# Kernel tuning notes

Measured on AMD Instinct MI355X. Metric: run time of the kernel, lower is better.

Reference implementation:

```python
import jax, jax.numpy as jnp
import numpy as np

EMB = 128
HEADS = 8
B = 8
T = 2048


def setup_inputs() -> dict:
    key = jax.random.key(0)
    ks = jax.random.split(key, 6)
    x = jax.random.normal(ks[0], (B, T, EMB), dtype=jnp.float32)
    # torch Linear(emb, heads*emb, bias=False): store as (in, out) so y = x @ W
    scale = 1.0 / np.sqrt(EMB)
    Wq = jax.random.uniform(ks[1], (EMB, HEADS * EMB), jnp.float32, -scale, scale)
    Wk = jax.random.uniform(ks[2], (EMB, HEADS * EMB), jnp.float32, -scale, scale)
    Wv = jax.random.uniform(ks[3], (EMB, HEADS * EMB), jnp.float32, -scale, scale)
    so = 1.0 / np.sqrt(HEADS * EMB)
    Wo = jax.random.uniform(ks[4], (HEADS * EMB, EMB), jnp.float32, -so, so)
    bo = jax.random.uniform(ks[5], (EMB,), jnp.float32, -so, so)
    return {"x": x, "Wq": Wq, "Wk": Wk, "Wv": Wv, "Wo": Wo, "bo": bo}


def reference(x, Wq, Wk, Wv, Wo, bo):
    b, t, e = x.shape
    h = HEADS
    q = (x @ Wq).reshape(b, t, h, e)  # [b,t,h,e]
    k = (x @ Wk).reshape(b, t, h, e)
    v = (x @ Wv).reshape(b, t, h, e)
    # scores: [b,h,q,k], scaled by sqrt(e) (per-head dim == emb here)
    scores = jnp.einsum('bqhe,bkhe->bhqk', q, k) / jnp.sqrt(jnp.asarray(e, x.dtype))
    attn = jax.nn.softmax(scores, axis=-1)
    out = jnp.einsum('bhqk,bkhe->bqhe', attn, v).reshape(b, t, h * e)
    return out @ Wo + bo
```

## Files before the change

kernel.cpp:

```cpp
#include <hip/hip_runtime.h>

using bf16x8 = __attribute__((ext_vector_type(8))) short;
using f32x4  = __attribute__((ext_vector_type(4))) float;

__device__ __forceinline__ ushort f2bf(float f) {
    union { float f; unsigned int u; } c; c.f = f;
    unsigned int u = c.u;
    u = (u + 0x7fffu + ((u >> 16) & 1u)) >> 16;
    return (ushort)u;
}

#if defined(__has_builtin)
#if __has_builtin(__builtin_amdgcn_cvt_pk_bf16_f32)
#define HAS_PK_BF16 1
#endif
#endif
__device__ __forceinline__ unsigned int pkbf(float a, float b) {
#ifdef HAS_PK_BF16
    typedef __bf16 bf2 __attribute__((ext_vector_type(2)));
    union { bf2 v; unsigned int u; } cv;
    cv.v = __builtin_amdgcn_cvt_pk_bf16_f32(a, b);
    return cv.u;
#else
    return (unsigned int)f2bf(a) | ((unsigned int)f2bf(b) << 16);
#endif
}

__device__ __forceinline__ void dma16(const ushort* g, ushort* l) {
    __builtin_amdgcn_global_load_lds(
        (const __attribute__((address_space(1))) unsigned int*)g,
        (__attribute__((address_space(3))) unsigned int*)l, 16, 0, 0);
}

constexpr int BB   = 8;
constexpr int HH   = 8;
constexpr int TT   = 2048;
constexpr int DD   = 128;
#define C2F (0.08838834764831845f * 1.4426950408889634f)

__global__ void prep_kernel(const float* __restrict__ x,
                            const float* __restrict__ Wq, const float* __restrict__ Wk,
                            const float* __restrict__ Wv, const float* __restrict__ Wo,
                            ushort* __restrict__ xb, ushort* __restrict__ WqkvT,
                            ushort* __restrict__ WoT) {
    int t = blockIdx.x * 256 + threadIdx.x;
    if (t < 524288) {
        float4 v = ((const float4*)x)[t];
        ushort4 o;
        o.x = f2bf(v.x); o.y = f2bf(v.y); o.z = f2bf(v.z); o.w = f2bf(v.w);
        ((ushort4*)xb)[t] = o;
    } else if (t < 524288 + 393216) {
        int i = t - 524288;
        int j = i >> 7, kk = i & 127;
        const float* W = (j < 1024) ? Wq : ((j < 2048) ? Wk : Wv);
        int jj = j & 1023;
        WqkvT[j * 128 + kk] = f2bf(W[kk * 1024 + jj]);
    } else {
        int i = t - 917504;
        int e = i >> 10, kk = i & 1023;
        WoT[e * 1024 + kk] = f2bf(Wo[kk * 128 + e]);
    }
}

__global__ __launch_bounds__(256, 2)
void qkv_gemm(const ushort* __restrict__ xb, const ushort* __restrict__ WqkvT,
              ushort* __restrict__ q, ushort* __restrict__ k, ushort* __restrict__ vt) {
    __shared__ ushort Al[128 * 136];
    __shared__ ushort Bl[128 * 136];
    const int tid = threadIdx.x;
    const int n0 = blockIdx.x * 128, m0 = blockIdx.y * 128;

    for (int s = tid; s < 2048; s += 256) {
        int row = s >> 4, oct = s & 15;
        *(uint4*)&Al[row * 136 + oct * 8] = *(const uint4*)&xb[m0 * 128 + s * 8];
        *(uint4*)&Bl[row * 136 + oct * 8] = *(const uint4*)&WqkvT[n0 * 128 + s * 8];
    }
    __syncthreads();

    const int w = tid >> 6, lane = tid & 63, l15 = lane & 15, g = lane >> 4;
    const int wm = (w & 1) * 64, wn = (w >> 1) * 64;
    f32x4 acc[4][4] = {};

#pragma unroll
    for (int ks = 0; ks < 4; ks++) {
        bf16x8 af[4], bfr[4];
#pragma unroll
        for (int mb = 0; mb < 4; mb++)
            af[mb] = *(const bf16x8*)&Al[(wm + mb * 16 + l15) * 136 + ks * 32 + g * 8];
#pragma unroll
        for (int nb = 0; nb < 4; nb++)
            bfr[nb] = *(const bf16x8*)&Bl[(wn + nb * 16 + l15) * 136 + ks * 32 + g * 8];
#pragma unroll
        for (int mb = 0; mb < 4; mb++)
#pragma unroll
            for (int nb = 0; nb < 4; nb++)
                acc[mb][nb] = __builtin_amdgcn_mfma_f32_16x16x32_bf16(af[mb], bfr[nb], acc[mb][nb], 0, 0, 0);
    }

    const int which = n0 >> 10;
    const int b = m0 >> 11;
    const int h = (n0 >> 7) & 7;
    const int bh = b * HH + h;
    if (which == 0) {
#pragma unroll
        for (int mb = 0; mb < 4; mb++)
#pragma unroll
            for (int nb = 0; nb < 4; nb++)
#pragma unroll
                for (int r = 0; r < 4; r++) {
                    int t = (m0 + wm + mb * 16 + g * 4 + r) & 2047;
                    int e = wn + nb * 16 + l15;
                    q[((size_t)bh * TT + t) * DD + e] = f2bf(acc[mb][nb][r]);
                }
    } else if (which == 1) {
#pragma unroll
        for (int mb = 0; mb < 4; mb++)
#pragma unroll
            for (int nb = 0; nb < 4; nb++)
#pragma unroll
                for (int r = 0; r < 4; r++) {
                    int t = (m0 + wm + mb * 16 + g * 4 + r) & 2047;
                    int e = wn + nb * 16 + l15;
                    int esw = ((((e >> 3) ^ (t & 7)) << 3) | (e & 7));
                    k[((size_t)bh * TT + t) * DD + esw] = f2bf(acc[mb][nb][r]);
                }
    } else {
        __syncthreads();
        ushort* Tl = Al;
#pragma unroll
        for (int mb = 0; mb < 4; mb++)
#pragma unroll
            for (int nb = 0; nb < 4; nb++)
#pragma unroll
                for (int r = 0; r < 4; r++)
                    Tl[(wn + nb * 16 + l15) * 136 + wm + mb * 16 + g * 4 + r] = f2bf(acc[mb][nb][r]);
        __syncthreads();
        const int c0 = (m0 & 2047) >> 5;
        for (int s = tid; s < 2048; s += 256) {
            int e = s >> 4, x = s & 15;
            int cl = x >> 2, pos = x & 3;
            int el = e & 15;
            int vsw = (el ^ (el >> 2)) & 3;
            int tsrc = cl * 32 + ((pos ^ vsw) * 8);
            uint4 val = *(const uint4*)&Tl[e * 136 + tsrc];
            *(uint4*)&vt[(size_t)(((bh * 64 + c0 + cl) * 128) + e) * 32 + pos * 8] = val;
        }
    }
}

__global__ __launch_bounds__(256, 2)
void attn_kernel(const ushort* __restrict__ q, const ushort* __restrict__ k,
                 const ushort* __restrict__ vt, ushort* __restrict__ ao) {
    __shared__ ushort Kl[2][32 * 128];
    __shared__ ushort Vl[2][128 * 32];
    __shared__ ushort Pl[4 * 64 * 32];

    const int idx = blockIdx.x;
    const int qt256 = idx & 7, h = (idx >> 3) & 7, b = idx >> 6;
    const int t0 = qt256 * 256;
    const int bh = b * HH + h;
    const ushort* qg  = q  + (size_t)bh * TT * DD;
    const ushort* kg  = k  + (size_t)bh * TT * DD;
    const ushort* vtg = vt + (size_t)bh * 64 * DD * 32;

    const int tid = threadIdx.x, w = tid >> 6, lane = tid & 63;
    const int l15 = lane & 15, g = lane >> 4;
    const int swk = l15 & 7;
    const int swv = (l15 ^ (l15 >> 2)) & 3;

    bf16x8 qf[4][4];
#pragma unroll
    for (int qt = 0; qt < 4; qt++)
#pragma unroll
        for (int ks = 0; ks < 4; ks++)
            qf[qt][ks] = *(const bf16x8*)&qg[(size_t)(t0 + w * 64 + qt * 16 + l15) * DD + ks * 32 + g * 8];

    const int seg = tid * 8;
#pragma unroll
    for (int j = 0; j < 2; j++) {
        dma16(kg  + seg + j * 2048, &Kl[0][seg + j * 2048]);
        dma16(vtg + seg + j * 2048, &Vl[0][seg + j * 2048]);
    }

    f32x4 o[4][8] = {};
    float ls[4] = {0.0f, 0.0f, 0.0f, 0.0f};

    for (int c = 0; c < 64; c++) {
        const int cur = c & 1;
        __syncthreads();

        if (c < 63) {
            const ushort* kn = kg  + (size_t)(c + 1) * 4096;
            const ushort* vn = vtg + (size_t)(c + 1) * 4096;
#pragma unroll
            for (int j = 0; j < 2; j++) {
                dma16(kn + seg + j * 2048, &Kl[cur ^ 1][seg + j * 2048]);
                dma16(vn + seg + j * 2048, &Vl[cur ^ 1][seg + j * 2048]);
            }
        }

#pragma unroll
        for (int kt = 0; kt < 2; kt++) {
            f32x4 st[4] = {};
#pragma unroll
            for (int ks = 0; ks < 4; ks++) {
                bf16x8 kf = *(const bf16x8*)&Kl[cur][(kt * 16 + l15) * 128 + (((ks * 4 + g) ^ swk) * 8)];
#pragma unroll
                for (int qt = 0; qt < 4; qt++)
                    st[qt] = __builtin_amdgcn_mfma_f32_16x16x32_bf16(kf, qf[qt][ks], st[qt], 0, 0, 0);
            }
            const int kb = 2 * kt + (g >> 1);
#pragma unroll
            for (int qt = 0; qt < 4; qt++) {
                float p0 = __builtin_amdgcn_exp2f(st[qt][0] * C2F);
                float p1 = __builtin_amdgcn_exp2f(st[qt][1] * C2F);
                float p2 = __builtin_amdgcn_exp2f(st[qt][2] * C2F);
                float p3 = __builtin_amdgcn_exp2f(st[qt][3] * C2F);
                ls[qt] += (p0 + p1) + (p2 + p3);
                uint2 pk;
                pk.x = pkbf(p0, p1);
                pk.y = pkbf(p2, p3);
                *(uint2*)&Pl[w * 2048 + (qt * 16 + l15) * 32 + ((kb ^ swv) * 8) + (g & 1) * 4] = pk;
            }
        }

        {
            bf16x8 pa[4];
#pragma unroll
            for (int qt = 0; qt < 4; qt++)
                pa[qt] = *(const bf16x8*)&Pl[w * 2048 + (qt * 16 + l15) * 32 + ((g ^ swv) * 8)];
#pragma unroll
            for (int eb = 0; eb < 8; eb++) {
                bf16x8 vb = *(const bf16x8*)&Vl[cur][(eb * 16 + l15) * 32 + ((g ^ swv) * 8)];
#pragma unroll
                for (int qt = 0; qt < 4; qt++)
                    o[qt][eb] = __builtin_amdgcn_mfma_f32_16x16x32_bf16(pa[qt], vb, o[qt][eb], 0, 0, 0);
            }
        }
    }

#pragma unroll
    for (int qt = 0; qt < 4; qt++) {
        float tot = ls[qt];
        tot += __shfl_xor(tot, 16);
        tot += __shfl_xor(tot, 32);
        float inv[4];
#pragma unroll
        for (int r = 0; r < 4; r++)
            inv[r] = 1.0f / __shfl(tot, g * 4 + r, 64);
#pragma unroll
        for (int eb = 0; eb < 8; eb++)
#pragma unroll
            for (int r = 0; r < 4; r++) {
                int m = t0 + w * 64 + qt * 16 + g * 4 + r;
                int col = h * 128 + eb * 16 + l15;
                ao[(size_t)(b * TT + m) * 1024 + col] = f2bf(o[qt][eb][r] * inv[r]);
            }
    }
}

__global__ __launch_bounds__(256, 2)
void outproj_gemm(const ushort* __restrict__ ao, const ushort* __restrict__ WoT,
                  const float* __restrict__ bo, float* __restrict__ out) {
    __shared__ ushort Al[64 * 72];
    __shared__ ushort Bl[64 * 72];
    const int tid = threadIdx.x;
    const int n0 = blockIdx.x * 64, m0 = blockIdx.y * 64;
    const int w = tid >> 6, lane = tid & 63, l15 = lane & 15, g = lane >> 4;
    const int wm = (w & 1) * 32, wn = (w >> 1) * 32;
    f32x4 acc[2][2] = {};

    for (int kc = 0; kc < 16; kc++) {
        int k0 = kc * 64;
        __syncthreads();
        for (int s = tid; s < 512; s += 256) {
            int row = s >> 3, oct = s & 7;
            *(uint4*)&Al[row * 72 + oct * 8] = *(const uint4*)&ao[(size_t)(m0 + row) * 1024 + k0 + oct * 8];
            *(uint4*)&Bl[row * 72 + oct * 8] = *(const uint4*)&WoT[(n0 + row) * 1024 + k0 + oct * 8];
        }
        __syncthreads();
#pragma unroll
        for (int ks = 0; ks < 2; ks++) {
            bf16x8 af[2], bfr[2];
#pragma unroll
            for (int mb = 0; mb < 2; mb++)
                af[mb] = *(const bf16x8*)&Al[(wm + mb * 16 + l15) * 72 + ks * 32 + g * 8];
#pragma unroll
            for (int nb = 0; nb < 2; nb++)
                bfr[nb] = *(const bf16x8*)&Bl[(wn + nb * 16 + l15) * 72 + ks * 32 + g * 8];
#pragma unroll
            for (int mb = 0; mb < 2; mb++)
#pragma unroll
                for (int nb = 0; nb < 2; nb++)
                    acc[mb][nb] = __builtin_amdgcn_mfma_f32_16x16x32_bf16(af[mb], bfr[nb], acc[mb][nb], 0, 0, 0);
        }
    }

#pragma unroll
    for (int mb = 0; mb < 2; mb++)
#pragma unroll
        for (int nb = 0; nb < 2; nb++) {
            int j = n0 + wn + nb * 16 + l15;
            float bias = bo[j];
#pragma unroll
            for (int r = 0; r < 4; r++) {
                int m = m0 + wm + mb * 16 + g * 4 + r;
                out[(size_t)m * 128 + j] = acc[mb][nb][r] + bias;
            }
        }
}

extern "C" void kernel_launch(void* const* d_in, const int* in_sizes, int n_in,
                              void* d_out, int out_size, void* d_ws, size_t ws_size,
                              hipStream_t stream) {
    const float* x  = (const float*)d_in[0];
    const float* Wq = (const float*)d_in[1];
    const float* Wk = (const float*)d_in[2];
    const float* Wv = (const float*)d_in[3];
    const float* Wo = (const float*)d_in[4];
    const float* bo = (const float*)d_in[5];
    float* out = (float*)d_out;

    char* ws = (char*)d_ws;
    ushort* xb    = (ushort*)(ws);
    ushort* WqkvT = (ushort*)(ws + 4194304);
    ushort* WoT   = (ushort*)(ws + 4980736);
    ushort* qb    = (ushort*)(ws + 5242880);
    ushort* kb    = (ushort*)(ws + 38797312);
    ushort* vtb   = (ushort*)(ws + 72351744);
    ushort* ao    = (ushort*)(ws + 105906176);

    prep_kernel<<<4096, 256, 0, stream>>>(x, Wq, Wk, Wv, Wo, xb, WqkvT, WoT);
    qkv_gemm<<<dim3(24, 128), 256, 0, stream>>>(xb, WqkvT, qb, kb, vtb);
    attn_kernel<<<512, 256, 0, stream>>>(qb, kb, vtb, ao);
    outproj_gemm<<<dim3(2, 256), 256, 0, stream>>>(ao, WoT, bo, out);
}
```

Before: 274.3 us.

## Switch attention to 32x32x16 MFMA with register-resident P via permlane32 swap

Rewrites the attention inner loop to use 32x32x16 bf16 MFMA tiles instead of 16x16x32, so the S-to-P accumulator layout can feed the PV MFMA directly after a permlane32 swap, removing the per-chunk LDS round trip for P. The softmax scale is folded into Q during the projection kernel, which removes a multiply per score. It also adds s_setprio around the MFMA sections and drops the P shared buffer, which reduces LDS usage. The risk is higher register pressure from the 16-wide accumulators and reliance on the permlane32 swap instruction layout being correct.

```diff
diff --git a/kernel.cpp b/kernel.cpp
--- a/kernel.cpp
+++ b/kernel.cpp
@@ -2,6 +2,7 @@
 
 using bf16x8 = __attribute__((ext_vector_type(8))) short;
 using f32x4  = __attribute__((ext_vector_type(4))) float;
+using f32x16 = __attribute__((ext_vector_type(16))) float;
 
 __device__ __forceinline__ ushort f2bf(float f) {
     union { float f; unsigned int u; } c; c.f = f;
@@ -13,6 +14,9 @@
 #if defined(__has_builtin)
 #if __has_builtin(__builtin_amdgcn_cvt_pk_bf16_f32)
 #define HAS_PK_BF16 1
+#endif
+#if __has_builtin(__builtin_amdgcn_permlane32_swap)
+#define HAS_PL32 1
 #endif
 #endif
 __device__ __forceinline__ unsigned int pkbf(float a, float b) {
@@ -23,6 +27,16 @@
     return cv.u;
 #else
     return (unsigned int)f2bf(a) | ((unsigned int)f2bf(b) << 16);
+#endif
+}
+
+__device__ __forceinline__ void pl32swap(unsigned &a, unsigned &b) {
+#ifdef HAS_PL32
+    typedef unsigned uint2v __attribute__((ext_vector_type(2)));
+    uint2v r = __builtin_amdgcn_permlane32_swap(a, b, false, false);
+    a = r.x; b = r.y;
+#else
+    asm volatile("v_permlane32_swap_b32 %0, %1" : "+v"(a), "+v"(b));
 #endif
 }
 
@@ -110,7 +124,7 @@
                 for (int r = 0; r < 4; r++) {
                     int t = (m0 + wm + mb * 16 + g * 4 + r) & 2047;
                     int e = wn + nb * 16 + l15;
-                    q[((size_t)bh * TT + t) * DD + e] = f2bf(acc[mb][nb][r]);
+                    q[((size_t)bh * TT + t) * DD + e] = f2bf(acc[mb][nb][r] * C2F);
                 }
     } else if (which == 1) {
 #pragma unroll
@@ -153,7 +167,6 @@
                  const ushort* __restrict__ vt, ushort* __restrict__ ao) {
     __shared__ ushort Kl[2][32 * 128];
     __shared__ ushort Vl[2][128 * 32];
-    __shared__ ushort Pl[4 * 64 * 32];
 
     const int idx = blockIdx.x;
     const int qt256 = idx & 7, h = (idx >> 3) & 7, b = idx >> 6;
@@ -164,16 +177,16 @@
     const ushort* vtg = vt + (size_t)bh * 64 * DD * 32;
 
     const int tid = threadIdx.x, w = tid >> 6, lane = tid & 63;
-    const int l15 = lane & 15, g = lane >> 4;
-    const int swk = l15 & 7;
+    const int l31 = lane & 31, hi = lane >> 5, l15 = lane & 15;
+    const int swk = lane & 7;
     const int swv = (l15 ^ (l15 >> 2)) & 3;
 
-    bf16x8 qf[4][4];
-#pragma unroll
-    for (int qt = 0; qt < 4; qt++)
-#pragma unroll
-        for (int ks = 0; ks < 4; ks++)
-            qf[qt][ks] = *(const bf16x8*)&qg[(size_t)(t0 + w * 64 + qt * 16 + l15) * DD + ks * 32 + g * 8];
+    bf16x8 qf[2][8];
+#pragma unroll
+    for (int qt = 0; qt < 2; qt++)
+#pragma unroll
+        for (int ks = 0; ks < 8; ks++)
+            qf[qt][ks] = *(const bf16x8*)&qg[(size_t)(t0 + w * 64 + qt * 32 + l31) * DD + ks * 16 + hi * 8];
 
     const int seg = tid * 8;
 #pragma unroll
@@ -182,8 +195,8 @@
         dma16(vtg + seg + j * 2048, &Vl[0][seg + j * 2048]);
     }
 
-    f32x4 o[4][8] = {};
-    float ls[4] = {0.0f, 0.0f, 0.0f, 0.0f};
+    f32x16 o[2][4] = {};
+    float ls[2] = {0.0f, 0.0f};
 
     for (int c = 0; c < 64; c++) {
         const int cur = c & 1;
@@ -199,63 +212,63 @@
             }
         }
 
-#pragma unroll
-        for (int kt = 0; kt < 2; kt++) {
-            f32x4 st[4] = {};
-#pragma unroll
-            for (int ks = 0; ks < 4; ks++) {
-                bf16x8 kf = *(const bf16x8*)&Kl[cur][(kt * 16 + l15) * 128 + (((ks * 4 + g) ^ swk) * 8)];
-#pragma unroll
-                for (int qt = 0; qt < 4; qt++)
-                    st[qt] = __builtin_amdgcn_mfma_f32_16x16x32_bf16(kf, qf[qt][ks], st[qt], 0, 0, 0);
+        f32x16 st0 = {}, st1 = {};
+        __builtin_amdgcn_s_setprio(1);
+#pragma unroll
+        for (int ks = 0; ks < 8; ks++) {
+            bf16x8 kf = *(const bf16x8*)&Kl[cur][l31 * 128 + (((ks * 2 + hi) ^ swk) * 8)];
+            st0 = __builtin_amdgcn_mfma_f32_32x32x16_bf16(kf, qf[0][ks], st0, 0, 0, 0);
+            st1 = __builtin_amdgcn_mfma_f32_32x32x16_bf16(kf, qf[1][ks], st1, 0, 0, 0);
+        }
+        __builtin_amdgcn_s_setprio(0);
+
+        bf16x8 pa00, pa01, pa10, pa11;
+        auto sm = [&](const f32x16 st, float& lsr, bf16x8& paA, bf16x8& paB) {
+            float p[16];
+#pragma unroll
+            for (int r = 0; r < 16; r++) p[r] = __builtin_amdgcn_exp2f(st[r]);
+            lsr += (((p[0] + p[1]) + (p[2] + p[3])) + ((p[4] + p[5]) + (p[6] + p[7])))
+                 + (((p[8] + p[9]) + (p[10] + p[11])) + ((p[12] + p[13]) + (p[14] + p[15])));
+            unsigned a0 = pkbf(p[0],  p[1]),  a1 = pkbf(p[2],  p[3]);
+            unsigned a2 = pkbf(p[4],  p[5]),  a3 = pkbf(p[6],  p[7]);
+            unsigned a4 = pkbf(p[8],  p[9]),  a5 = pkbf(p[10], p[11]);
+            unsigned a6 = pkbf(p[12], p[13]), a7 = pkbf(p[14], p[15]);
+            pl32swap(a0, a2); pl32swap(a1, a3);
+            pl32swap(a4, a6); pl32swap(a5, a7);
+            union { unsigned u[4]; bf16x8 v; } A, B;
+            A.u[0] = a0; A.u[1] = a1; A.u[2] = a2; A.u[3] = a3;
+            B.u[0] = a4; B.u[1] = a5; B.u[2] = a6; B.u[3] = a7;
+            paA = A.v; paB = B.v;
+        };
+        sm(st0, ls[0], pa00, pa01);
+        sm(st1, ls[1], pa10, pa11);
+
+        __builtin_amdgcn_s_setprio(1);
+#pragma unroll
+        for (int et = 0; et < 4; et++) {
+#pragma unroll
+            for (int ks2 = 0; ks2 < 2; ks2++) {
+                bf16x8 vb = *(const bf16x8*)&Vl[cur][(et * 32 + l31) * 32 + (((ks2 * 2 + hi) ^ swv) * 8)];
+                o[0][et] = __builtin_amdgcn_mfma_f32_32x32x16_bf16(ks2 ? pa01 : pa00, vb, o[0][et], 0, 0, 0);
+                o[1][et] = __builtin_amdgcn_mfma_f32_32x32x16_bf16(ks2 ? pa11 : pa10, vb, o[1][et], 0, 0, 0);
             }
-            const int kb = 2 * kt + (g >> 1);
-#pragma unroll
-            for (int qt = 0; qt < 4; qt++) {
-                float p0 = __builtin_amdgcn_exp2f(st[qt][0] * C2F);
-                float p1 = __builtin_amdgcn_exp2f(st[qt][1] * C2F);
-                float p2 = __builtin_amdgcn_exp2f(st[qt][2] * C2F);
-                float p3 = __builtin_amdgcn_exp2f(st[qt][3] * C2F);
-                ls[qt] += (p0 + p1) + (p2 + p3);
-                uint2 pk;
-                pk.x = pkbf(p0, p1);
-                pk.y = pkbf(p2, p3);
-                *(uint2*)&Pl[w * 2048 + (qt * 16 + l15) * 32 + ((kb ^ swv) * 8) + (g & 1) * 4] = pk;
-            }
-        }
-
-        {
-            bf16x8 pa[4];
-#pragma unroll
-            for (int qt = 0; qt < 4; qt++)
-                pa[qt] = *(const bf16x8*)&Pl[w * 2048 + (qt * 16 + l15) * 32 + ((g ^ swv) * 8)];
-#pragma unroll
-            for (int eb = 0; eb < 8; eb++) {
-                bf16x8 vb = *(const bf16x8*)&Vl[cur][(eb * 16 + l15) * 32 + ((g ^ swv) * 8)];
-#pragma unroll
-                for (int qt = 0; qt < 4; qt++)
-                    o[qt][eb] = __builtin_amdgcn_mfma_f32_16x16x32_bf16(pa[qt], vb, o[qt][eb], 0, 0, 0);
-            }
-        }
-    }
-
-#pragma unroll
-    for (int qt = 0; qt < 4; qt++) {
-        float tot = ls[qt];
-        tot += __shfl_xor(tot, 16);
-        tot += __shfl_xor(tot, 32);
-        float inv[4];
-#pragma unroll
-        for (int r = 0; r < 4; r++)
-            inv[r] = 1.0f / __shfl(tot, g * 4 + r, 64);
-#pragma unroll
-        for (int eb = 0; eb < 8; eb++)
-#pragma unroll
-            for (int r = 0; r < 4; r++) {
-                int m = t0 + w * 64 + qt * 16 + g * 4 + r;
-                int col = h * 128 + eb * 16 + l15;
-                ao[(size_t)(b * TT + m) * 1024 + col] = f2bf(o[qt][eb][r] * inv[r]);
-            }
+        }
+        __builtin_amdgcn_s_setprio(0);
+    }
+
+    const size_t aobase = (size_t)(b * TT) * 1024 + h * 128;
+#pragma unroll
+    for (int qt = 0; qt < 2; qt++) {
+        float tot = ls[qt] + __shfl_xor(ls[qt], 32);
+#pragma unroll
+        for (int r = 0; r < 16; r++) {
+            int ql = (r & 3) + 8 * (r >> 2) + 4 * hi;
+            float inv = 1.0f / __shfl(tot, ql, 64);
+            int m = t0 + w * 64 + qt * 32 + ql;
+#pragma unroll
+            for (int et = 0; et < 4; et++)
+                ao[aobase + (size_t)m * 1024 + et * 32 + l31] = f2bf(o[qt][et][r] * inv);
+        }
     }
 }
 
```

New measurement: 271.7 us. No clear change (-1.0%).
